# Optimization experiments

Measured on AMD Instinct MI355X. Metric: run time of the kernel, lower is better.

Reference implementation:

```python
import jax, jax.numpy as jnp
import numpy as np

EPS = 1e-12  # matches torch F.normalize / CosineSimilarity eps scale (1e-12 / 1e-8; vectors are unit so effect is negligible)


def setup_inputs() -> dict:
    key = jax.random.key(0)
    X = jax.random.normal(key, (64, 1024, 128), dtype=jnp.float32)
    return {"X": X}


def reference(X) -> jnp.ndarray:
    # F.normalize(X, dim=-1)
    Xn = X / jnp.maximum(jnp.linalg.norm(X, axis=-1, keepdims=True), EPS)
    # CosineSimilarity on unit vectors == batched X @ X^T  -> [B, scale, scale]
    S = jnp.einsum("bsd,btd->bst", Xn, Xn)
    # MSE vs ones per batch, averaged over batch == global mean of (S-1)^2
    return jnp.mean((S - 1.0) ** 2)
```

## Files before the change

### kernel.cpp

```cpp
#include <hip/hip_runtime.h>
#include <hip/hip_bf16.h>


#define BATCH 64
#define SEQ   1024
#define DIM   128

typedef short short8  __attribute__((ext_vector_type(8)));
typedef float floatx4 __attribute__((ext_vector_type(4)));

__device__ __forceinline__ unsigned bf16rne(float x) {
    unsigned u = __builtin_bit_cast(unsigned, x);
    return (u + 0x7FFFu + ((u >> 16) & 1u)) >> 16;
}

#define XNT_B  0
#define VP_B   16777216
#define RES_B  (VP_B + 1024 * 256 * 4)


__global__ __launch_bounds__(256, 4)
void kA_norm_t(const float* __restrict__ X, unsigned* __restrict__ XnT,
               float* __restrict__ vpartA) {
    __shared__ __align__(16) float lds[64][132];
    const int t     = threadIdx.x;
    const int wg    = blockIdx.x;
    const int b     = wg & 63, chunk = wg >> 6;
    const int sl    = t >> 2, q = t & 3;
    const int f     = t & 127, sh = t >> 7;
    const int rb    = f >> 4, l15 = f & 15;

    const float4* rp = (const float4*)(
        X + ((size_t)(b * SEQ + chunk * 64 + sl) * DIM + q * 32));
    float4 g[8];
#pragma unroll
    for (int k = 0; k < 8; ++k) g[k] = rp[k];

    float ssq = 0.0f;
#pragma unroll
    for (int k = 0; k < 8; ++k)
        ssq += g[k].x * g[k].x + g[k].y * g[k].y +
               g[k].z * g[k].z + g[k].w * g[k].w;
    ssq += __shfl_xor(ssq, 1);
    ssq += __shfl_xor(ssq, 2);
    const float inv = rsqrtf(fmaxf(ssq, 1e-24f));

#pragma unroll
    for (int k = 0; k < 8; ++k) {
        float4 n;
        n.x = g[k].x * inv; n.y = g[k].y * inv;
        n.z = g[k].z * inv; n.w = g[k].w * inv;
        *(float4*)&lds[sl][q * 32 + k * 4] = n;
    }
    __syncthreads();

    float vacc = 0.0f;
    float v[32];
#pragma unroll
    for (int j = 0; j < 32; ++j) {
        v[j] = lds[sh * 32 + j][f];
        vacc += v[j];
    }
    unsigned pk[16];
#pragma unroll
    for (int p = 0; p < 16; ++p)
        pk[p] = bf16rne(v[2 * p]) | (bf16rne(v[2 * p + 1]) << 16);

    const int kk = chunk * 2 + sh;
    uint4* op = (uint4*)(XnT + (((size_t)((b * 8 + rb) * 32 + kk)) << 8));
#pragma unroll
    for (int k = 0; k < 4; ++k)
        op[k * 16 + l15] = make_uint4(pk[4 * k], pk[4 * k + 1],
                                      pk[4 * k + 2], pk[4 * k + 3]);

    vpartA[(size_t)wg * 256 + t] = vacc;
}

__global__ __launch_bounds__(256, 2)
void kB_gram(const unsigned* __restrict__ XnT, const float* __restrict__ vpartA,
             float* __restrict__ res) {
    const int t    = threadIdx.x;
    const int wg   = blockIdx.x;
    const int b    = wg & 63, band = wg >> 6;
    const int lane = t & 63, w = t >> 6;

    const unsigned* Ab  = XnT + (((size_t)((b * 8 + band) * 32)) << 8) + lane * 4;
    const unsigned* B0b = XnT + (((size_t)((b * 8 + 2 * w) * 32)) << 8) + lane * 4;
    const unsigned* B1b = XnT + (((size_t)((b * 8 + 2 * w + 1) * 32)) << 8) + lane * 4;

    floatx4 acc0 = {0.f, 0.f, 0.f, 0.f}, acc1 = {0.f, 0.f, 0.f, 0.f};
#pragma unroll 8
    for (int kk = 0; kk < 32; ++kk) {
        short8 a  = *(const short8*)(Ab  + (kk << 8));
        short8 b0 = *(const short8*)(B0b + (kk << 8));
        short8 b1 = *(const short8*)(B1b + (kk << 8));
        acc0 = __builtin_amdgcn_mfma_f32_16x16x32_bf16(a, b0, acc0, 0, 0, 0);
        acc1 = __builtin_amdgcn_mfma_f32_16x16x32_bf16(a, b1, acc1, 0, 0, 0);
    }

    float s = acc0[0] * acc0[0] + acc0[1] * acc0[1] +
              acc0[2] * acc0[2] + acc0[3] * acc0[3] +
              acc1[0] * acc1[0] + acc1[1] * acc1[1] +
              acc1[2] * acc1[2] + acc1[3] * acc1[3];

    if (band == 0 && t < DIM) {
        float vv = 0.0f;
#pragma unroll
        for (int c = 0; c < 16; ++c) {
            const float* p = vpartA + (size_t)(c * 64 + b) * 256;
            vv += p[t] + p[t + 128];
        }
        s -= 2.0f * vv * vv;
    }

#pragma unroll
    for (int m = 1; m < 64; m <<= 1) s += __shfl_xor(s, m);
    __shared__ float wq[4];
    if (lane == 0) wq[w] = s;
    __syncthreads();
    if (t == 0) res[wg] = wq[0] + wq[1] + wq[2] + wq[3];
}

__global__ __launch_bounds__(256)
void kF_final(const float* __restrict__ res, float* __restrict__ out) {
    const int t = threadIdx.x;
    float s = res[t] + res[t + 256];
#pragma unroll
    for (int m = 1; m < 64; m <<= 1) s += __shfl_xor(s, m);
    __shared__ float wq[4];
    if ((t & 63) == 0) wq[t >> 6] = s;
    __syncthreads();
    if (t == 0)
        out[0] = (wq[0] + wq[1] + wq[2] + wq[3]) * (1.0f / 67108864.0f) + 1.0f;
}

extern "C" void kernel_launch(void* const* d_in, const int* in_sizes, int n_in,
                              void* d_out, int out_size, void* d_ws, size_t ws_size,
                              hipStream_t stream) {
    const float* X = (const float*)d_in[0];
    char* ws = (char*)d_ws;
    unsigned* XnT  = (unsigned*)(ws + XNT_B);
    float* vpartA  = (float*)(ws + VP_B);
    float* res     = (float*)(ws + RES_B);

    kA_norm_t<<<1024, 256, 0, stream>>>(X, XnT, vpartA);
    kB_gram<<<512, 256, 0, stream>>>(XnT, vpartA, res);
    kF_final<<<1, 256, 0, stream>>>(res, (float*)d_out);
}
```

Before: 85.90 us.

## Store normalized transposed X as scaled FP8 and use FP8 MFMA for Gram

Quantizes the normalized, transposed activations to FP8 e4m3 with a x16 scale instead of bf16, halving the intermediate buffer written by the normalize kernel and read by the Gram kernel. The Gram kernel switches to the 16x16x32 fp8 MFMA and rescales the squared accumulations by 1/65536, with the column-sum partials rescaled to match. This cuts memory traffic in both kernels but lowers precision of the Gram entries, which could push the scalar loss outside tolerance.

Result: faster. 81.78 us (-4.8%).

```diff
diff --git a/kernel.cpp b/kernel.cpp
--- a/kernel.cpp
+++ b/kernel.cpp
@@ -6,16 +6,35 @@
 #define SEQ   1024
 #define DIM   128
 
-typedef short short8  __attribute__((ext_vector_type(8)));
 typedef float floatx4 __attribute__((ext_vector_type(4)));
 
-__device__ __forceinline__ unsigned bf16rne(float x) {
+#if defined(__has_builtin)
+#if __has_builtin(__builtin_amdgcn_cvt_pk_fp8_f32)
+#define HAVE_CVT_FP8 1
+#endif
+#endif
+
+__device__ __forceinline__ unsigned f2e4m3(float x) {
     unsigned u = __builtin_bit_cast(unsigned, x);
-    return (u + 0x7FFFu + ((u >> 16) & 1u)) >> 16;
+    unsigned r = u + 0x7FFFFu + ((u >> 20) & 1u);
+    unsigned t = (r >> 20) & 0x7FFu;
+    unsigned mag = (t >= 968u) ? (t - 960u) : 0u;
+    return mag | ((u >> 24) & 0x80u);
+}
+
+__device__ __forceinline__ unsigned pack4_fp8(const float* v) {
+#ifdef HAVE_CVT_FP8
+    int w = __builtin_amdgcn_cvt_pk_fp8_f32(v[0], v[1], 0, false);
+    w = __builtin_amdgcn_cvt_pk_fp8_f32(v[2], v[3], w, true);
+    return (unsigned)w;
+#else
+    return f2e4m3(v[0]) | (f2e4m3(v[1]) << 8) |
+           (f2e4m3(v[2]) << 16) | (f2e4m3(v[3]) << 24);
+#endif
 }
 
 #define XNT_B  0
-#define VP_B   16777216
+#define VP_B   8388608
 #define RES_B  (VP_B + 1024 * 256 * 4)
 
 
@@ -43,13 +62,13 @@
                g[k].z * g[k].z + g[k].w * g[k].w;
     ssq += __shfl_xor(ssq, 1);
     ssq += __shfl_xor(ssq, 2);
-    const float inv = rsqrtf(fmaxf(ssq, 1e-24f));
+    const float inv16 = rsqrtf(fmaxf(ssq, 1e-24f)) * 16.0f;
 
 #pragma unroll
     for (int k = 0; k < 8; ++k) {
         float4 n;
-        n.x = g[k].x * inv; n.y = g[k].y * inv;
-        n.z = g[k].z * inv; n.w = g[k].w * inv;
+        n.x = g[k].x * inv16; n.y = g[k].y * inv16;
+        n.z = g[k].z * inv16; n.w = g[k].w * inv16;
         *(float4*)&lds[sl][q * 32 + k * 4] = n;
     }
     __syncthreads();
@@ -61,19 +80,18 @@
         v[j] = lds[sh * 32 + j][f];
         vacc += v[j];
     }
-    unsigned pk[16];
+    unsigned pk[8];
 #pragma unroll
-    for (int p = 0; p < 16; ++p)
-        pk[p] = bf16rne(v[2 * p]) | (bf16rne(v[2 * p + 1]) << 16);
+    for (int p = 0; p < 8; ++p) pk[p] = pack4_fp8(v + 4 * p);
 
     const int kk = chunk * 2 + sh;
-    uint4* op = (uint4*)(XnT + (((size_t)((b * 8 + rb) * 32 + kk)) << 8));
+    uint2* op = (uint2*)((char*)XnT +
+                         ((size_t)((b * 8 + rb) * 32 + kk) << 9));
 #pragma unroll
-    for (int k = 0; k < 4; ++k)
-        op[k * 16 + l15] = make_uint4(pk[4 * k], pk[4 * k + 1],
-                                      pk[4 * k + 2], pk[4 * k + 3]);
+    for (int kqi = 0; kqi < 4; ++kqi)
+        op[kqi * 16 + l15] = make_uint2(pk[2 * kqi], pk[2 * kqi + 1]);
 
-    vpartA[(size_t)wg * 256 + t] = vacc;
+    vpartA[(size_t)wg * 256 + t] = vacc * 0.0625f;
 }
 
 __global__ __launch_bounds__(256, 2)
@@ -84,24 +102,27 @@
     const int b    = wg & 63, band = wg >> 6;
     const int lane = t & 63, w = t >> 6;
 
-    const unsigned* Ab  = XnT + (((size_t)((b * 8 + band) * 32)) << 8) + lane * 4;
-    const unsigned* B0b = XnT + (((size_t)((b * 8 + 2 * w) * 32)) << 8) + lane * 4;
-    const unsigned* B1b = XnT + (((size_t)((b * 8 + 2 * w + 1) * 32)) << 8) + lane * 4;
+    const long* Ab  = (const long*)((const char*)XnT +
+                      ((size_t)((b * 8 + band) * 32) << 9)) + lane;
+    const long* B0b = (const long*)((const char*)XnT +
+                      ((size_t)((b * 8 + 2 * w) * 32) << 9)) + lane;
+    const long* B1b = (const long*)((const char*)XnT +
+                      ((size_t)((b * 8 + 2 * w + 1) * 32) << 9)) + lane;
 
     floatx4 acc0 = {0.f, 0.f, 0.f, 0.f}, acc1 = {0.f, 0.f, 0.f, 0.f};
 #pragma unroll 8
     for (int kk = 0; kk < 32; ++kk) {
-        short8 a  = *(const short8*)(Ab  + (kk << 8));
-        short8 b0 = *(const short8*)(B0b + (kk << 8));
-        short8 b1 = *(const short8*)(B1b + (kk << 8));
-        acc0 = __builtin_amdgcn_mfma_f32_16x16x32_bf16(a, b0, acc0, 0, 0, 0);
-        acc1 = __builtin_amdgcn_mfma_f32_16x16x32_bf16(a, b1, acc1, 0, 0, 0);
+        long a  = Ab[kk * 64];
+        long b0 = B0b[kk * 64];
+        long b1 = B1b[kk * 64];
+        acc0 = __builtin_amdgcn_mfma_f32_16x16x32_fp8_fp8(a, b0, acc0, 0, 0, 0);
+        acc1 = __builtin_amdgcn_mfma_f32_16x16x32_fp8_fp8(a, b1, acc1, 0, 0, 0);
     }
 
-    float s = acc0[0] * acc0[0] + acc0[1] * acc0[1] +
-              acc0[2] * acc0[2] + acc0[3] * acc0[3] +
-              acc1[0] * acc1[0] + acc1[1] * acc1[1] +
-              acc1[2] * acc1[2] + acc1[3] * acc1[3];
+    float s = (acc0[0] * acc0[0] + acc0[1] * acc0[1] +
+               acc0[2] * acc0[2] + acc0[3] * acc0[3] +
+               acc1[0] * acc1[0] + acc1[1] * acc1[1] +
+               acc1[2] * acc1[2] + acc1[3] * acc1[3]) * (1.0f / 65536.0f);
 
     if (band == 0 && t < DIM) {
         float vv = 0.0f;
```
